# Performance work log

Hardware: AMD Instinct MI355X
Metric: run time of the kernel (lower is better)

Reference implementation:

```python
import jax, jax.numpy as jnp
import numpy as np

GROUPSIZE = 4      # g: multivariate group size (d = groupsize - 2)
NB_GROUPS = 48     # f: number of expert groups / filters
CHANNELS = 128     # c: signal channels fed to the L operator
SCALE = 0.999
SLOPE = 1.0        # model_params['scaling']
LAMB_INIT = 0.1
EPS_OMEGA_INIT = -2.0


def proj_l1(x):
    """Euclidean projection onto the unit l1 ball along axis 1. x: [B,G,F,H,W]."""
    ax = jnp.abs(x)
    s = -jnp.sort(-ax, axis=1)                      # descending |x|
    cssv = jnp.cumsum(s, axis=1) - 1.0
    G = x.shape[1]
    k = jnp.arange(1, G + 1, dtype=x.dtype).reshape(1, G, 1, 1, 1)
    cond = s * k > cssv
    rho = jnp.sum(cond, axis=1, keepdims=True)       # number of active coords
    theta = jnp.take_along_axis(cssv, rho - 1, axis=1) / rho.astype(x.dtype)
    theta = jnp.maximum(theta, 0.0)
    proj = jnp.sign(x) * jnp.maximum(ax - theta, 0.0)
    inside = jnp.sum(ax, axis=1, keepdims=True) <= 1.0
    return jnp.where(inside, x, proj)


def _forward(x_noisy, sigma, Q_param, taus_param, lamb, eps_omega,
             mu_w1, mu_b1, mu_w2, mu_b2, mu_w3, mu_b3, Wf, n_iter):
    lamb_e = jnp.exp(lamb)
    eps_e = jnp.exp(eps_omega)

    # --- Q normalization + spectral norms (cached once per forward) ---
    Q = Q_param / jnp.maximum(jnp.sum(jnp.abs(Q_param), axis=2, keepdims=True), 1.0)
    Q_norms = jnp.linalg.svd(Q, compute_uv=False)[:, 0].reshape(-1, 1, 1)  # [F,1,1]
    Q_eff = Q / Q_norms ** 2
    taus = jnp.exp(jax.nn.relu(taus_param))          # [1,1,F,1,1]

    # --- per-batch noise-adaptive scaling via small MLP ---
    h = jax.nn.relu((sigma * 20.0 - 2.0) @ mu_w1 + mu_b1)
    h = jax.nn.relu(h @ mu_w2 + mu_b2)
    h = h @ mu_w3 + mu_b3                            # [B,F]
    scaling = jax.nn.relu(h * 0.05 + sigma) * SLOPE + 1e-9
    scaling = scaling.reshape(-1, 1, scaling.shape[-1], 1, 1)  # [B,1,F,1,1]

    def moreau(x):
        g = proj_l1(x)
        cost = jnp.max(jnp.abs(x - g), axis=1) + 0.5 * jnp.sum(g * g, axis=1)
        cost = cost[:, None]                         # [B,1,F,H,W]
        g = g + eps_e * x
        cost = cost + eps_e * 0.5 * jnp.sqrt(jnp.sum(x * x, axis=1, keepdims=True))
        return g, cost

    def activation(x):
        gc, cc = moreau(x)
        # orient: scale * einsum('flg,bgfhw->blfhw', Q/Q_norms^2, x), then /taus
        y = SCALE * jnp.einsum('flg,bgfhw->blfhw', Q_eff, x) / taus
        gcc, ccc = moreau(y)
        # unorient: scale * einsum with Q^T  (Q^T[f,l,g] = Q[f,g,l])
        gcc = SCALE * jnp.einsum('fgl,bgfhw->blfhw', Q, gcc)
        ccc = Q_norms ** 2 * (taus * ccc)
        return lamb_e * (gc - gcc), lamb_e * (cc - ccc)

    def reconstruct(x):
        Lx = jnp.einsum('gfc,bchw->bgfhw', Wf, x) / scaling
        g, cost = activation(Lx)
        g = jnp.einsum('gfc,bgfhw->bchw', Wf, g * scaling)   # adjoint L^T
        cost = jnp.sum(cost * scaling ** 2, axis=(1, 2, 3, 4))
        g = (x - x_noisy + g) / (1.0 + lamb_e * (1.0 + eps_e))
        cost = cost + 0.5 * jnp.sum((x - x_noisy) ** 2, axis=(1, 2, 3))
        return g, cost

    def step(x, _):
        g, _c = reconstruct(x)
        return x - g, None

    x_final, _ = jax.lax.scan(jax.checkpoint(step), x_noisy, jnp.arange(n_iter))
    return x_final


def setup_inputs() -> dict:
    key = jax.random.key(0)
    ks = jax.random.split(key, 8)
    B, C, H, W = 2, CHANNELS, 128, 128
    F_, G = NB_GROUPS, GROUPSIZE
    x_noisy = jax.random.normal(ks[0], (B, C, H, W), jnp.float32)
    sigma = jax.random.uniform(ks[1], (B, 1), jnp.float32)
    Q_param = jax.random.uniform(ks[2], (F_, G, G), jnp.float32) - 0.5
    taus_param = (LAMB_INIT / 2.0) * jnp.ones((1, 1, F_, 1, 1), jnp.float32)
    lamb = jnp.float32(LAMB_INIT)
    eps_omega = jnp.float32(EPS_OMEGA_INIT)
    mu_w1 = jax.random.normal(ks[3], (1, F_), jnp.float32)
    mu_b1 = jnp.zeros((F_,), jnp.float32)
    mu_w2 = jax.random.normal(ks[4], (F_, F_), jnp.float32) / np.float32(np.sqrt(F_))
    mu_b2 = jnp.zeros((F_,), jnp.float32)
    mu_w3 = jax.random.normal(ks[5], (F_, F_), jnp.float32) / np.float32(np.sqrt(F_))
    mu_b3 = jnp.zeros((F_,), jnp.float32)
    Wf = jax.random.normal(ks[6], (G, F_, C), jnp.float32) / np.float32(np.sqrt(C))
    return dict(x_noisy=x_noisy, sigma=sigma, Q_param=Q_param, taus_param=taus_param,
                lamb=lamb, eps_omega=eps_omega, mu_w1=mu_w1, mu_b1=mu_b1,
                mu_w2=mu_w2, mu_b2=mu_b2, mu_w3=mu_w3, mu_b3=mu_b3, Wf=Wf, n_iter=10)


def reference(x_noisy, sigma, Q_param, taus_param, lamb, eps_omega,
              mu_w1, mu_b1, mu_w2, mu_b2, mu_w3, mu_b3, Wf, n_iter):
    return _forward(x_noisy, sigma, Q_param, taus_param, lamb, eps_omega,
                    mu_w1, mu_b1, mu_w2, mu_b2, mu_w3, mu_b3, Wf, n_iter)
```

## Files before the change

kernel.cpp:

```cpp
#include <hip/hip_runtime.h>
#include <math.h>

#define F_ 48
#define C_ 128
#define HW 16384
#define SCALE_C 0.999f
#define TPB 256

typedef __attribute__((ext_vector_type(8))) short short8;
typedef __attribute__((ext_vector_type(4))) float floatx4;

#define P1_U 0
#define P2_U 98304
#define QEQN_F 98304
#define MISC_F (QEQN_F + 1536)
#define SINV_F (MISC_F + 2)
#define SLAM_F (SINV_F + 96)

#define XS 152
#define AS 104
#define QS 36

__device__ __forceinline__ unsigned short f2bf(float f) {
    unsigned u = __float_as_uint(f);
    unsigned r = u + 0x7fffu + ((u >> 16) & 1u);
    return (unsigned short)(r >> 16);
}
__device__ __forceinline__ float bf2f(unsigned short h) {
    return __uint_as_float(((unsigned)h) << 16);
}

__global__ void setup_math(const float* __restrict__ sigma,
                           const float* __restrict__ Qp,
                           const float* __restrict__ taus_p,
                           const float* __restrict__ lamb,
                           const float* __restrict__ eps_om,
                           const float* __restrict__ mw1, const float* __restrict__ mb1,
                           const float* __restrict__ mw2, const float* __restrict__ mb2,
                           const float* __restrict__ mw3, const float* __restrict__ mb3,
                           float* __restrict__ wsf)
{
    const int tid = threadIdx.x;
    if (tid < F_) {
        const int f = tid;
        float Qm[4][4];
        for (int g = 0; g < 4; ++g) {
            float s = 0.f;
            for (int l = 0; l < 4; ++l) s += fabsf(Qp[f * 16 + g * 4 + l]);
            float d = fmaxf(s, 1.0f);
            for (int l = 0; l < 4; ++l) Qm[g][l] = Qp[f * 16 + g * 4 + l] / d;
        }
        double A[4][4];
        for (int i = 0; i < 4; ++i)
            for (int j = 0; j < 4; ++j) {
                double s = 0.0;
                for (int g = 0; g < 4; ++g) s += (double)Qm[g][i] * (double)Qm[g][j];
                A[i][j] = s;
            }
        double M[4][4];
        for (int i = 0; i < 4; ++i) for (int j = 0; j < 4; ++j) M[i][j] = A[i][j];
        for (int it = 0; it < 30; ++it) {
            double T[4][4]; double mx = 0.0;
            for (int i = 0; i < 4; ++i)
                for (int j = 0; j < 4; ++j) {
                    double s = 0.0;
                    for (int k = 0; k < 4; ++k) s += M[i][k] * M[k][j];
                    T[i][j] = s;
                    double a = fabs(s); if (a > mx) mx = a;
                }
            if (mx < 1e-300) break;
            double inv = 1.0 / mx;
            for (int i = 0; i < 4; ++i) for (int j = 0; j < 4; ++j) M[i][j] = T[i][j] * inv;
        }
        int jb = 0; double bn = -1.0;
        for (int j = 0; j < 4; ++j) {
            double nn = 0.0;
            for (int i = 0; i < 4; ++i) nn += M[i][j] * M[i][j];
            if (nn > bn) { bn = nn; jb = j; }
        }
        double v[4]; for (int i = 0; i < 4; ++i) v[i] = M[i][jb];
        double Av[4];
        for (int i = 0; i < 4; ++i) {
            double s = 0.0;
            for (int j = 0; j < 4; ++j) s += A[i][j] * v[j];
            Av[i] = s;
        }
        double vv = 0.0, vav = 0.0;
        for (int i = 0; i < 4; ++i) { vv += v[i] * v[i]; vav += v[i] * Av[i]; }
        float lamf = (float)((vv > 0.0) ? (vav / vv) : 0.0);
        float tau = expf(fmaxf(taus_p[f], 0.0f));
        float qsv = SCALE_C / tau;
        for (int l = 0; l < 4; ++l)
            for (int g = 0; g < 4; ++g)
                wsf[QEQN_F + f * 32 + l * 4 + g] = qsv * Qm[l][g] / lamf;
        for (int g = 0; g < 4; ++g)
            for (int l = 0; l < 4; ++l)
                wsf[QEQN_F + f * 32 + 16 + g * 4 + l] = SCALE_C * Qm[g][l];
    }
    if (tid >= 48 && tid < 50) {
        const int b = tid - 48;
        float lamb_e = expf(lamb[0]);
        float sg = sigma[b];
        float t = sg * 20.0f - 2.0f;
        float h1[F_], h2[F_];
        for (int j = 0; j < F_; ++j) h1[j] = fmaxf(t * mw1[j] + mb1[j], 0.0f);
        for (int j = 0; j < F_; ++j) {
            float s = mb2[j];
            for (int k = 0; k < F_; ++k) s += h1[k] * mw2[k * F_ + j];
            h2[j] = fmaxf(s, 0.0f);
        }
        for (int j = 0; j < F_; ++j) {
            float s = mb3[j];
            for (int k = 0; k < F_; ++k) s += h2[k] * mw3[k * F_ + j];
            float sc = fmaxf(s * 0.05f + sg, 0.0f) + 1e-9f;
            wsf[SINV_F + b * F_ + j] = 1.0f / sc;
            wsf[SLAM_F + b * F_ + j] = lamb_e * sc;
        }
    }
    if (tid == 50) {
        float lamb_e = expf(lamb[0]);
        float eps_e = expf(eps_om[0]);
        wsf[MISC_F + 0] = eps_e;
        wsf[MISC_F + 1] = 1.0f / (1.0f + lamb_e * (1.0f + eps_e));
    }
}

__global__ void setup_pack(const float* __restrict__ Wf, float* __restrict__ wsf)
{
    unsigned short* wsu = (unsigned short*)wsf;
    const int gtid = blockIdx.x * TPB + threadIdx.x;
    for (int i = gtid; i < 49152; i += gridDim.x * TPB) {
        if (i < 24576) {
            int j = i & 7, lane = (i >> 3) & 63;
            int t = i >> 9;
            int ks = t & 3, mt = t >> 2;
            int m = lane & 15, q = lane >> 4;
            int r = mt * 16 + m;
            int c = ks * 32 + q * 8 + j;
            int f = r >> 2, g = r & 3;
            float w = Wf[(g * F_ + f) * C_ + c];
#pragma unroll
            for (int b = 0; b < 2; ++b) {
                float v = w * wsf[SINV_F + b * F_ + f];
                unsigned short h = (unsigned short)(__float_as_uint(v) >> 16);
                float lo = v - bf2f(h);
                unsigned short l = (unsigned short)(__float_as_uint(lo) >> 16);
                wsu[P1_U + ((((b * 2 + 0) * 12 + mt) * 4 + ks) * 64 + lane) * 8 + j] = h;
                wsu[P1_U + ((((b * 2 + 1) * 12 + mt) * 4 + ks) * 64 + lane) * 8 + j] = l;
            }
        } else {
            int ii = i - 24576;
            int j = ii & 7, lane = (ii >> 3) & 63;
            int t = ii >> 9;
            int ks = t % 6, cmt = t / 6;
            int m = lane & 15, q = lane >> 4;
            int cch = cmt * 16 + m;
            int r = ks * 32 + q * 8 + j;
            int f = r >> 2, g = r & 3;
            float w = Wf[(g * F_ + f) * C_ + cch];
#pragma unroll
            for (int b = 0; b < 2; ++b) {
                float v = w * wsf[SLAM_F + b * F_ + f];
                unsigned short h = (unsigned short)(__float_as_uint(v) >> 16);
                float lo = v - bf2f(h);
                unsigned short l = (unsigned short)(__float_as_uint(lo) >> 16);
                wsu[P2_U + ((((b * 2 + 0) * 8 + cmt) * 6 + ks) * 64 + lane) * 8 + j] = h;
                wsu[P2_U + ((((b * 2 + 1) * 8 + cmt) * 6 + ks) * 64 + lane) * 8 + j] = l;
            }
        }
    }
}

__device__ __forceinline__ void proj4(const float v[4], float o[4]) {
    float a0 = fabsf(v[0]), a1 = fabsf(v[1]), a2 = fabsf(v[2]), a3 = fabsf(v[3]);
    float sum = a0 + a1 + a2 + a3;
    float t0 = fmaxf(a0, a1), u0 = fminf(a0, a1);
    float t1 = fmaxf(a2, a3), u1 = fminf(a2, a3);
    float s0 = fmaxf(t0, t1), m0 = fminf(t0, t1);
    float m1 = fmaxf(u0, u1), s3 = fminf(u0, u1);
    float s1 = fmaxf(m1, m0), s2 = fminf(m1, m0);
    float c2 = s0 + s1, c3 = c2 + s2, c4 = c3 + s3;
    float th = s0 - 1.0f, rh = 1.0f;
    if (s1 * 2.0f > c2 - 1.0f) { th = c2 - 1.0f; rh = 2.0f; }
    if (s2 * 3.0f > c3 - 1.0f) { th = c3 - 1.0f; rh = 3.0f; }
    if (s3 * 4.0f > c4 - 1.0f) { th = c4 - 1.0f; rh = 4.0f; }
    float theta = fmaxf(th / rh, 0.0f);
    bool inside = (sum <= 1.0f);
#pragma unroll
    for (int g = 0; g < 4; ++g) {
        float ag = fabsf(v[g]);
        float pg = copysignf(fmaxf(ag - theta, 0.0f), v[g]);
        o[g] = inside ? v[g] : pg;
    }
}

__global__ __launch_bounds__(TPB, 4) void mfoe_main(
    const float* __restrict__ xnoisy,
    const float* __restrict__ wsf,
    float* __restrict__ out,
    const int* __restrict__ n_iter_p)
{
    __shared__ __align__(16) unsigned short sXH[32 * XS];
    __shared__ __align__(16) unsigned short sXL[32 * XS];
    __shared__ __align__(16) unsigned short sACT[32 * AS];
    __shared__ __align__(16) float sQ[F_ * QS];

    const int tid = threadIdx.x;
    const int lane = tid & 63;
    const int wv = __builtin_amdgcn_readfirstlane(tid >> 6);
    const int n = lane & 15;
    const int q = lane >> 4;
    const int blk = blockIdx.x;
    const int b = blk >> 9;
    const int pix0 = (blk & 511) << 5;

    const float* __restrict__ xin = xnoisy + b * (C_ * HW) + pix0;
    float* __restrict__ oimg = out + b * (C_ * HW) + pix0;
    const unsigned short* __restrict__ wsu = (const unsigned short*)wsf;
    const int niter = *n_iter_p;

    if (niter == 0) {
        for (int i = tid; i < C_ * 32; i += TPB) {
            int p = i & 31, c = i >> 5;
            oimg[c * HW + p] = xin[c * HW + p];
        }
        return;
    }

    for (int i = tid; i < C_ * 32; i += TPB) {
        int p = i & 31, c = i >> 5;
        float v = xin[c * HW + p];
        unsigned short h = (unsigned short)(__float_as_uint(v) >> 16);
        float lo = v - bf2f(h);
        sXH[p * XS + c] = h;
        sXL[p * XS + c] = (unsigned short)(__float_as_uint(lo) >> 16);
    }
    for (int i = tid; i < F_ * 32; i += TPB)
        sQ[(i >> 5) * QS + (i & 31)] = wsf[QEQN_F + i];

    float xnr[16];
#pragma unroll
    for (int j = 0; j < 4; ++j) {
        int jw = wv * 4 + j, cmt = jw >> 1, nt = jw & 1;
        int p = nt * 16 + n;
#pragma unroll
        for (int reg = 0; reg < 4; ++reg)
            xnr[j * 4 + reg] = xin[(cmt * 16 + q * 4 + reg) * HW + p];
    }
    const float eps_e = wsf[MISC_F + 0];
    const float invden = wsf[MISC_F + 1];

    for (int it = 0; it < niter; ++it) {
        floatx4 acc2[4];
#pragma unroll
        for (int j = 0; j < 4; ++j) acc2[j] = (floatx4){0.f, 0.f, 0.f, 0.f};

#pragma unroll 1
        for (int h = 0; h < 2; ++h) {
            __syncthreads();
#pragma unroll 1
            for (int j = 0; j < 3; ++j) {
                int jw = wv * 3 + j, mtl = jw >> 1, nt = jw & 1;
                int mt = h * 6 + mtl;
                int p = nt * 16 + n;
                floatx4 acc = (floatx4){0.f, 0.f, 0.f, 0.f};
                const short8* aHp = (const short8*)(wsu + P1_U + (((b * 2 + 0) * 12 + mt) * 4) * 512 + lane * 8);
                const short8* aLp = (const short8*)(wsu + P1_U + (((b * 2 + 1) * 12 + mt) * 4) * 512 + lane * 8);
#pragma unroll
                for (int ks = 0; ks < 4; ++ks) {
                    short8 aH = aHp[ks * 64];
                    short8 aL = aLp[ks * 64];
                    short8 bH = *(const short8*)&sXH[p * XS + ks * 32 + q * 8];
                    short8 bL = *(const short8*)&sXL[p * XS + ks * 32 + q * 8];
                    acc = __builtin_amdgcn_mfma_f32_16x16x32_bf16(aH, bH, acc, 0, 0, 0);
                    acc = __builtin_amdgcn_mfma_f32_16x16x32_bf16(aH, bL, acc, 0, 0, 0);
                    acc = __builtin_amdgcn_mfma_f32_16x16x32_bf16(aL, bH, acc, 0, 0, 0);
                }
                int f = h * 24 + mtl * 4 + q;
                float qv[32];
#pragma unroll
                for (int k = 0; k < 8; ++k)
                    *(floatx4*)&qv[4 * k] = *(const floatx4*)&sQ[f * QS + 4 * k];
                float v[4] = {acc[0], acc[1], acc[2], acc[3]};
                float pv[4]; proj4(v, pv);
                float y[4];
#pragma unroll
                for (int l = 0; l < 4; ++l)
                    y[l] = fmaf(qv[l * 4 + 0], v[0], fmaf(qv[l * 4 + 1], v[1],
                           fmaf(qv[l * 4 + 2], v[2], qv[l * 4 + 3] * v[3])));
                float py[4]; proj4(y, py);
                float m2[4];
#pragma unroll
                for (int g = 0; g < 4; ++g) m2[g] = fmaf(eps_e, y[g], py[g]);
                unsigned pk0, pk1;
                {
                    float a0, a1;
                    float gcc0 = fmaf(qv[16 + 0], m2[0], fmaf(qv[16 + 4], m2[1],
                                 fmaf(qv[16 + 8], m2[2], qv[16 + 12] * m2[3])));
                    a0 = fmaf(eps_e, v[0], pv[0]) - gcc0;
                    float gcc1 = fmaf(qv[17 + 0], m2[0], fmaf(qv[17 + 4], m2[1],
                                 fmaf(qv[17 + 8], m2[2], qv[17 + 12] * m2[3])));
                    a1 = fmaf(eps_e, v[1], pv[1]) - gcc1;
                    pk0 = ((unsigned)f2bf(a1) << 16) | f2bf(a0);
                    float gcc2 = fmaf(qv[18 + 0], m2[0], fmaf(qv[18 + 4], m2[1],
                                 fmaf(qv[18 + 8], m2[2], qv[18 + 12] * m2[3])));
                    a0 = fmaf(eps_e, v[2], pv[2]) - gcc2;
                    float gcc3 = fmaf(qv[19 + 0], m2[0], fmaf(qv[19 + 4], m2[1],
                                 fmaf(qv[19 + 8], m2[2], qv[19 + 12] * m2[3])));
                    a1 = fmaf(eps_e, v[3], pv[3]) - gcc3;
                    pk1 = ((unsigned)f2bf(a1) << 16) | f2bf(a0);
                }
                unsigned long long pk = ((unsigned long long)pk1 << 32) | pk0;
                *(unsigned long long*)&sACT[p * AS + mtl * 16 + q * 4] = pk;
            }
            __syncthreads();
#pragma unroll
            for (int j = 0; j < 4; ++j) {
                int jw = wv * 4 + j, cmt = jw >> 1, nt = jw & 1;
                int p = nt * 16 + n;
                const short8* a2H = (const short8*)(wsu + P2_U + (((b * 2 + 0) * 8 + cmt) * 6 + h * 3) * 512 + lane * 8);
                const short8* a2L = (const short8*)(wsu + P2_U + (((b * 2 + 1) * 8 + cmt) * 6 + h * 3) * 512 + lane * 8);
                floatx4 a = acc2[j];
#pragma unroll
                for (int ksl = 0; ksl < 3; ++ksl) {
                    short8 aH = a2H[ksl * 64];
                    short8 aL = a2L[ksl * 64];
                    short8 bA = *(const short8*)&sACT[p * AS + ksl * 32 + q * 8];
                    a = __builtin_amdgcn_mfma_f32_16x16x32_bf16(aH, bA, a, 0, 0, 0);
                    a = __builtin_amdgcn_mfma_f32_16x16x32_bf16(aL, bA, a, 0, 0, 0);
                }
                acc2[j] = a;
            }
        }
        const bool last = (it == niter - 1);
#pragma unroll
        for (int j = 0; j < 4; ++j) {
            int jw = wv * 4 + j, cmt = jw >> 1, nt = jw & 1;
            int p = nt * 16 + n;
            int cb = cmt * 16 + q * 4;
            unsigned long long oh = *(const unsigned long long*)&sXH[p * XS + cb];
            unsigned long long ol = *(const unsigned long long*)&sXL[p * XS + cb];
            unsigned long long nh = 0ull, nl = 0ull;
#pragma unroll
            for (int reg = 0; reg < 4; ++reg) {
                float xo = bf2f((unsigned short)(oh >> (16 * reg))) +
                           bf2f((unsigned short)(ol >> (16 * reg)));
                float nx = xo - (xo - xnr[j * 4 + reg] + acc2[j][reg]) * invden;
                if (last) oimg[(cb + reg) * HW + p] = nx;
                unsigned short hh = (unsigned short)(__float_as_uint(nx) >> 16);
                float lo = nx - bf2f(hh);
                unsigned short ll = (unsigned short)(__float_as_uint(lo) >> 16);
                nh |= ((unsigned long long)hh) << (16 * reg);
                nl |= ((unsigned long long)ll) << (16 * reg);
            }
            *(unsigned long long*)&sXH[p * XS + cb] = nh;
            *(unsigned long long*)&sXL[p * XS + cb] = nl;
        }
    }
}

extern "C" void kernel_launch(void* const* d_in, const int* in_sizes, int n_in,
                              void* d_out, int out_size, void* d_ws, size_t ws_size,
                              hipStream_t stream) {
    const float* x_noisy = (const float*)d_in[0];
    const float* sigma   = (const float*)d_in[1];
    const float* Qp      = (const float*)d_in[2];
    const float* taus_p  = (const float*)d_in[3];
    const float* lamb    = (const float*)d_in[4];
    const float* eps_om  = (const float*)d_in[5];
    const float* mw1     = (const float*)d_in[6];
    const float* mb1     = (const float*)d_in[7];
    const float* mw2     = (const float*)d_in[8];
    const float* mb2     = (const float*)d_in[9];
    const float* mw3     = (const float*)d_in[10];
    const float* mb3     = (const float*)d_in[11];
    const float* Wf      = (const float*)d_in[12];
    const int*   n_iter  = (const int*)d_in[13];
    float* out = (float*)d_out;
    float* ws  = (float*)d_ws;

    hipLaunchKernelGGL(setup_math, dim3(1), dim3(64), 0, stream,
                       sigma, Qp, taus_p, lamb, eps_om,
                       mw1, mb1, mw2, mb2, mw3, mb3, ws);
    hipLaunchKernelGGL(setup_pack, dim3(192), dim3(TPB), 0, stream, Wf, ws);
    hipLaunchKernelGGL(mfoe_main, dim3(1024), dim3(TPB), 0, stream,
                       x_noisy, ws, out, n_iter);
}
```

Baseline: 333.1 us.

## Merge setup kernels and process all filter groups in one activation pass

Two setup kernels are merged into one. Each block recomputes the small per-batch MLP scaling into shared memory, and block 0 alone writes the Q tables, which removes one launch. In the main loop the split over two halves of the 48 filters is removed. All 12 M-tiles are computed into a wider activation buffer in LDS (AS 104→200), followed by a single 6-step K loop for the second GEMM. This cuts barriers per iteration from four to two, at the cost of more LDS per block, which may lower occupancy.

Result: slower. 452.4 us (+35.8%).

```diff
diff --git a/kernel.cpp b/kernel.cpp
--- a/kernel.cpp
+++ b/kernel.cpp
@@ -9,16 +9,14 @@
 
 typedef __attribute__((ext_vector_type(8))) short short8;
 typedef __attribute__((ext_vector_type(4))) float floatx4;
+typedef __attribute__((ext_vector_type(2))) unsigned int uint2v;
 
 #define P1_U 0
 #define P2_U 98304
 #define QEQN_F 98304
 #define MISC_F (QEQN_F + 1536)
-#define SINV_F (MISC_F + 2)
-#define SLAM_F (SINV_F + 96)
-
 #define XS 152
-#define AS 104
+#define AS 200
 #define QS 36
 
 __device__ __forceinline__ unsigned short f2bf(float f) {
@@ -30,73 +28,22 @@
     return __uint_as_float(((unsigned)h) << 16);
 }
 
-__global__ void setup_math(const float* __restrict__ sigma,
-                           const float* __restrict__ Qp,
-                           const float* __restrict__ taus_p,
-                           const float* __restrict__ lamb,
-                           const float* __restrict__ eps_om,
-                           const float* __restrict__ mw1, const float* __restrict__ mb1,
-                           const float* __restrict__ mw2, const float* __restrict__ mb2,
-                           const float* __restrict__ mw3, const float* __restrict__ mb3,
-                           float* __restrict__ wsf)
+__global__ void setup_all(const float* __restrict__ sigma,
+                          const float* __restrict__ Qp,
+                          const float* __restrict__ taus_p,
+                          const float* __restrict__ lamb,
+                          const float* __restrict__ eps_om,
+                          const float* __restrict__ mw1, const float* __restrict__ mb1,
+                          const float* __restrict__ mw2, const float* __restrict__ mb2,
+                          const float* __restrict__ mw3, const float* __restrict__ mb3,
+                          const float* __restrict__ Wf,
+                          float* __restrict__ wsf)
 {
+    __shared__ float sInv[2][F_];
+    __shared__ float sLam[2][F_];
     const int tid = threadIdx.x;
-    if (tid < F_) {
-        const int f = tid;
-        float Qm[4][4];
-        for (int g = 0; g < 4; ++g) {
-            float s = 0.f;
-            for (int l = 0; l < 4; ++l) s += fabsf(Qp[f * 16 + g * 4 + l]);
-            float d = fmaxf(s, 1.0f);
-            for (int l = 0; l < 4; ++l) Qm[g][l] = Qp[f * 16 + g * 4 + l] / d;
-        }
-        double A[4][4];
-        for (int i = 0; i < 4; ++i)
-            for (int j = 0; j < 4; ++j) {
-                double s = 0.0;
-                for (int g = 0; g < 4; ++g) s += (double)Qm[g][i] * (double)Qm[g][j];
-                A[i][j] = s;
-            }
-        double M[4][4];
-        for (int i = 0; i < 4; ++i) for (int j = 0; j < 4; ++j) M[i][j] = A[i][j];
-        for (int it = 0; it < 30; ++it) {
-            double T[4][4]; double mx = 0.0;
-            for (int i = 0; i < 4; ++i)
-                for (int j = 0; j < 4; ++j) {
-                    double s = 0.0;
-                    for (int k = 0; k < 4; ++k) s += M[i][k] * M[k][j];
-                    T[i][j] = s;
-                    double a = fabs(s); if (a > mx) mx = a;
-                }
-            if (mx < 1e-300) break;
-            double inv = 1.0 / mx;
-            for (int i = 0; i < 4; ++i) for (int j = 0; j < 4; ++j) M[i][j] = T[i][j] * inv;
-        }
-        int jb = 0; double bn = -1.0;
-        for (int j = 0; j < 4; ++j) {
-            double nn = 0.0;
-            for (int i = 0; i < 4; ++i) nn += M[i][j] * M[i][j];
-            if (nn > bn) { bn = nn; jb = j; }
-        }
-        double v[4]; for (int i = 0; i < 4; ++i) v[i] = M[i][jb];
-        double Av[4];
-        for (int i = 0; i < 4; ++i) {
-            double s = 0.0;
-            for (int j = 0; j < 4; ++j) s += A[i][j] * v[j];
-            Av[i] = s;
-        }
-        double vv = 0.0, vav = 0.0;
-        for (int i = 0; i < 4; ++i) { vv += v[i] * v[i]; vav += v[i] * Av[i]; }
-        float lamf = (float)((vv > 0.0) ? (vav / vv) : 0.0);
-        float tau = expf(fmaxf(taus_p[f], 0.0f));
-        float qsv = SCALE_C / tau;
-        for (int l = 0; l < 4; ++l)
-            for (int g = 0; g < 4; ++g)
-                wsf[QEQN_F + f * 32 + l * 4 + g] = qsv * Qm[l][g] / lamf;
-        for (int g = 0; g < 4; ++g)
-            for (int l = 0; l < 4; ++l)
-                wsf[QEQN_F + f * 32 + 16 + g * 4 + l] = SCALE_C * Qm[g][l];
-    }
+    unsigned short* wsu = (unsigned short*)wsf;
+
     if (tid >= 48 && tid < 50) {
         const int b = tid - 48;
         float lamb_e = expf(lamb[0]);
@@ -113,23 +60,77 @@
             float s = mb3[j];
             for (int k = 0; k < F_; ++k) s += h2[k] * mw3[k * F_ + j];
             float sc = fmaxf(s * 0.05f + sg, 0.0f) + 1e-9f;
-            wsf[SINV_F + b * F_ + j] = 1.0f / sc;
-            wsf[SLAM_F + b * F_ + j] = lamb_e * sc;
-        }
-    }
-    if (tid == 50) {
-        float lamb_e = expf(lamb[0]);
-        float eps_e = expf(eps_om[0]);
-        wsf[MISC_F + 0] = eps_e;
-        wsf[MISC_F + 1] = 1.0f / (1.0f + lamb_e * (1.0f + eps_e));
-    }
-}
-
-__global__ void setup_pack(const float* __restrict__ Wf, float* __restrict__ wsf)
-{
-    unsigned short* wsu = (unsigned short*)wsf;
-    const int gtid = blockIdx.x * TPB + threadIdx.x;
-    for (int i = gtid; i < 49152; i += gridDim.x * TPB) {
+            sInv[b][j] = 1.0f / sc;
+            sLam[b][j] = lamb_e * sc;
+        }
+    }
+    if (blockIdx.x == 0) {
+        if (tid < F_) {
+            const int f = tid;
+            float Qm[4][4];
+            for (int g = 0; g < 4; ++g) {
+                float s = 0.f;
+                for (int l = 0; l < 4; ++l) s += fabsf(Qp[f * 16 + g * 4 + l]);
+                float d = fmaxf(s, 1.0f);
+                for (int l = 0; l < 4; ++l) Qm[g][l] = Qp[f * 16 + g * 4 + l] / d;
+            }
+            double A[4][4];
+            for (int i = 0; i < 4; ++i)
+                for (int j = 0; j < 4; ++j) {
+                    double s = 0.0;
+                    for (int g = 0; g < 4; ++g) s += (double)Qm[g][i] * (double)Qm[g][j];
+                    A[i][j] = s;
+                }
+            double M[4][4];
+            for (int i = 0; i < 4; ++i) for (int j = 0; j < 4; ++j) M[i][j] = A[i][j];
+            for (int it = 0; it < 30; ++it) {
+                double T[4][4]; double mx = 0.0;
+                for (int i = 0; i < 4; ++i)
+                    for (int j = 0; j < 4; ++j) {
+                        double s = 0.0;
+                        for (int k = 0; k < 4; ++k) s += M[i][k] * M[k][j];
+                        T[i][j] = s;
+                        double a = fabs(s); if (a > mx) mx = a;
+                    }
+                if (mx < 1e-300) break;
+                double inv = 1.0 / mx;
+                for (int i = 0; i < 4; ++i) for (int j = 0; j < 4; ++j) M[i][j] = T[i][j] * inv;
+            }
+            int jb = 0; double bn = -1.0;
+            for (int j = 0; j < 4; ++j) {
+                double nn = 0.0;
+                for (int i = 0; i < 4; ++i) nn += M[i][j] * M[i][j];
+                if (nn > bn) { bn = nn; jb = j; }
+            }
+            double v[4]; for (int i = 0; i < 4; ++i) v[i] = M[i][jb];
+            double Av[4];
+            for (int i = 0; i < 4; ++i) {
+                double s = 0.0;
+                for (int j = 0; j < 4; ++j) s += A[i][j] * v[j];
+                Av[i] = s;
+            }
+            double vv = 0.0, vav = 0.0;
+            for (int i = 0; i < 4; ++i) { vv += v[i] * v[i]; vav += v[i] * Av[i]; }
+            float lamf = (float)((vv > 0.0) ? (vav / vv) : 0.0);
+            float tau = expf(fmaxf(taus_p[f], 0.0f));
+            float qsv = SCALE_C / tau;
+            for (int l = 0; l < 4; ++l)
+                for (int g = 0; g < 4; ++g)
+                    wsf[QEQN_F + f * 32 + l * 4 + g] = qsv * Qm[l][g] / lamf;
+            for (int g = 0; g < 4; ++g)
+                for (int l = 0; l < 4; ++l)
+                    wsf[QEQN_F + f * 32 + 16 + g * 4 + l] = SCALE_C * Qm[g][l];
+        }
+        if (tid == 50) {
+            float lamb_e = expf(lamb[0]);
+            float eps_e = expf(eps_om[0]);
+            wsf[MISC_F + 0] = eps_e;
+            wsf[MISC_F + 1] = 1.0f / (1.0f + lamb_e * (1.0f + eps_e));
+        }
+    }
+    __syncthreads();
+
+    for (int i = blockIdx.x * TPB + tid; i < 49152; i += gridDim.x * TPB) {
         if (i < 24576) {
             int j = i & 7, lane = (i >> 3) & 63;
             int t = i >> 9;
@@ -141,7 +142,7 @@
             float w = Wf[(g * F_ + f) * C_ + c];
 #pragma unroll
             for (int b = 0; b < 2; ++b) {
-                float v = w * wsf[SINV_F + b * F_ + f];
+                float v = w * sInv[b][f];
                 unsigned short h = (unsigned short)(__float_as_uint(v) >> 16);
                 float lo = v - bf2f(h);
                 unsigned short l = (unsigned short)(__float_as_uint(lo) >> 16);
@@ -160,7 +161,7 @@
             float w = Wf[(g * F_ + f) * C_ + cch];
 #pragma unroll
             for (int b = 0; b < 2; ++b) {
-                float v = w * wsf[SLAM_F + b * F_ + f];
+                float v = w * sLam[b][f];
                 unsigned short h = (unsigned short)(__float_as_uint(v) >> 16);
                 float lo = v - bf2f(h);
                 unsigned short l = (unsigned short)(__float_as_uint(lo) >> 16);
@@ -251,86 +252,80 @@
     const float invden = wsf[MISC_F + 1];
 
     for (int it = 0; it < niter; ++it) {
+        __syncthreads();
+#pragma unroll 1
+        for (int j = 0; j < 6; ++j) {
+            int jw = wv * 6 + j, mt = jw >> 1, nt = jw & 1;
+            int p = nt * 16 + n;
+            floatx4 acc = (floatx4){0.f, 0.f, 0.f, 0.f};
+            const short8* aHp = (const short8*)(wsu + P1_U + (((b * 2 + 0) * 12 + mt) * 4) * 512 + lane * 8);
+            const short8* aLp = (const short8*)(wsu + P1_U + (((b * 2 + 1) * 12 + mt) * 4) * 512 + lane * 8);
+#pragma unroll
+            for (int ks = 0; ks < 4; ++ks) {
+                short8 aH = aHp[ks * 64];
+                short8 aL = aLp[ks * 64];
+                short8 bH = *(const short8*)&sXH[p * XS + ks * 32 + q * 8];
+                short8 bL = *(const short8*)&sXL[p * XS + ks * 32 + q * 8];
+                acc = __builtin_amdgcn_mfma_f32_16x16x32_bf16(aH, bH, acc, 0, 0, 0);
+                acc = __builtin_amdgcn_mfma_f32_16x16x32_bf16(aH, bL, acc, 0, 0, 0);
+                acc = __builtin_amdgcn_mfma_f32_16x16x32_bf16(aL, bH, acc, 0, 0, 0);
+            }
+            int f = mt * 4 + q;
+            float qv[32];
+#pragma unroll
+            for (int k = 0; k < 8; ++k)
+                *(floatx4*)&qv[4 * k] = *(const floatx4*)&sQ[f * QS + 4 * k];
+            float v[4] = {acc[0], acc[1], acc[2], acc[3]};
+            float pv[4]; proj4(v, pv);
+            float y[4];
+#pragma unroll
+            for (int l = 0; l < 4; ++l)
+                y[l] = fmaf(qv[l * 4 + 0], v[0], fmaf(qv[l * 4 + 1], v[1],
+                       fmaf(qv[l * 4 + 2], v[2], qv[l * 4 + 3] * v[3])));
+            float py[4]; proj4(y, py);
+            float m2[4];
+#pragma unroll
+            for (int g = 0; g < 4; ++g) m2[g] = fmaf(eps_e, y[g], py[g]);
+            unsigned pk0, pk1;
+            {
+                float a0, a1;
+                float gcc0 = fmaf(qv[16 + 0], m2[0], fmaf(qv[16 + 4], m2[1],
+                             fmaf(qv[16 + 8], m2[2], qv[16 + 12] * m2[3])));
+                a0 = fmaf(eps_e, v[0], pv[0]) - gcc0;
+                float gcc1 = fmaf(qv[17 + 0], m2[0], fmaf(qv[17 + 4], m2[1],
+                             fmaf(qv[17 + 8], m2[2], qv[17 + 12] * m2[3])));
+                a1 = fmaf(eps_e, v[1], pv[1]) - gcc1;
+                pk0 = ((unsigned)f2bf(a1) << 16) | f2bf(a0);
+                float gcc2 = fmaf(qv[18 + 0], m2[0], fmaf(qv[18 + 4], m2[1],
+                             fmaf(qv[18 + 8], m2[2], qv[18 + 12] * m2[3])));
+                a0 = fmaf(eps_e, v[2], pv[2]) - gcc2;
+                float gcc3 = fmaf(qv[19 + 0], m2[0], fmaf(qv[19 + 4], m2[1],
+                             fmaf(qv[19 + 8], m2[2], qv[19 + 12] * m2[3])));
+                a1 = fmaf(eps_e, v[3], pv[3]) - gcc3;
+                pk1 = ((unsigned)f2bf(a1) << 16) | f2bf(a0);
+            }
+            *(uint2v*)&sACT[p * AS + mt * 16 + q * 4] = (uint2v){pk0, pk1};
+        }
+        __syncthreads();
         floatx4 acc2[4];
 #pragma unroll
         for (int j = 0; j < 4; ++j) acc2[j] = (floatx4){0.f, 0.f, 0.f, 0.f};
-
-#pragma unroll 1
-        for (int h = 0; h < 2; ++h) {
-            __syncthreads();
-#pragma unroll 1
-            for (int j = 0; j < 3; ++j) {
-                int jw = wv * 3 + j, mtl = jw >> 1, nt = jw & 1;
-                int mt = h * 6 + mtl;
-                int p = nt * 16 + n;
-                floatx4 acc = (floatx4){0.f, 0.f, 0.f, 0.f};
-                const short8* aHp = (const short8*)(wsu + P1_U + (((b * 2 + 0) * 12 + mt) * 4) * 512 + lane * 8);
-                const short8* aLp = (const short8*)(wsu + P1_U + (((b * 2 + 1) * 12 + mt) * 4) * 512 + lane * 8);
-#pragma unroll
-                for (int ks = 0; ks < 4; ++ks) {
-                    short8 aH = aHp[ks * 64];
-                    short8 aL = aLp[ks * 64];
-                    short8 bH = *(const short8*)&sXH[p * XS + ks * 32 + q * 8];
-                    short8 bL = *(const short8*)&sXL[p * XS + ks * 32 + q * 8];
-                    acc = __builtin_amdgcn_mfma_f32_16x16x32_bf16(aH, bH, acc, 0, 0, 0);
-                    acc = __builtin_amdgcn_mfma_f32_16x16x32_bf16(aH, bL, acc, 0, 0, 0);
-                    acc = __builtin_amdgcn_mfma_f32_16x16x32_bf16(aL, bH, acc, 0, 0, 0);
-                }
-                int f = h * 24 + mtl * 4 + q;
-                float qv[32];
-#pragma unroll
-                for (int k = 0; k < 8; ++k)
-                    *(floatx4*)&qv[4 * k] = *(const floatx4*)&sQ[f * QS + 4 * k];
-                float v[4] = {acc[0], acc[1], acc[2], acc[3]};
-                float pv[4]; proj4(v, pv);
-                float y[4];
-#pragma unroll
-                for (int l = 0; l < 4; ++l)
-                    y[l] = fmaf(qv[l * 4 + 0], v[0], fmaf(qv[l * 4 + 1], v[1],
-                           fmaf(qv[l * 4 + 2], v[2], qv[l * 4 + 3] * v[3])));
-                float py[4]; proj4(y, py);
-                float m2[4];
-#pragma unroll
-                for (int g = 0; g < 4; ++g) m2[g] = fmaf(eps_e, y[g], py[g]);
-                unsigned pk0, pk1;
-                {
-                    float a0, a1;
-                    float gcc0 = fmaf(qv[16 + 0], m2[0], fmaf(qv[16 + 4], m2[1],
-                                 fmaf(qv[16 + 8], m2[2], qv[16 + 12] * m2[3])));
-                    a0 = fmaf(eps_e, v[0], pv[0]) - gcc0;
-                    float gcc1 = fmaf(qv[17 + 0], m2[0], fmaf(qv[17 + 4], m2[1],
-                                 fmaf(qv[17 + 8], m2[2], qv[17 + 12] * m2[3])));
-                    a1 = fmaf(eps_e, v[1], pv[1]) - gcc1;
-                    pk0 = ((unsigned)f2bf(a1) << 16) | f2bf(a0);
-                    float gcc2 = fmaf(qv[18 + 0], m2[0], fmaf(qv[18 + 4], m2[1],
-                                 fmaf(qv[18 + 8], m2[2], qv[18 + 12] * m2[3])));
-                    a0 = fmaf(eps_e, v[2], pv[2]) - gcc2;
-                    float gcc3 = fmaf(qv[19 + 0], m2[0], fmaf(qv[19 + 4], m2[1],
-                                 fmaf(qv[19 + 8], m2[2], qv[19 + 12] * m2[3])));
-                    a1 = fmaf(eps_e, v[3], pv[3]) - gcc3;
-                    pk1 = ((unsigned)f2bf(a1) << 16) | f2bf(a0);
-                }
-                unsigned long long pk = ((unsigned long long)pk1 << 32) | pk0;
-                *(unsigned long long*)&sACT[p * AS + mtl * 16 + q * 4] = pk;
-            }
-            __syncthreads();
-#pragma unroll
-            for (int j = 0; j < 4; ++j) {
-                int jw = wv * 4 + j, cmt = jw >> 1, nt = jw & 1;
-                int p = nt * 16 + n;
-                const short8* a2H = (const short8*)(wsu + P2_U + (((b * 2 + 0) * 8 + cmt) * 6 + h * 3) * 512 + lane * 8);
-                const short8* a2L = (const short8*)(wsu + P2_U + (((b * 2 + 1) * 8 + cmt) * 6 + h * 3) * 512 + lane * 8);
-                floatx4 a = acc2[j];
-#pragma unroll
-                for (int ksl = 0; ksl < 3; ++ksl) {
-                    short8 aH = a2H[ksl * 64];
-                    short8 aL = a2L[ksl * 64];
-                    short8 bA = *(const short8*)&sACT[p * AS + ksl * 32 + q * 8];
-                    a = __builtin_amdgcn_mfma_f32_16x16x32_bf16(aH, bA, a, 0, 0, 0);
-                    a = __builtin_amdgcn_mfma_f32_16x16x32_bf16(aL, bA, a, 0, 0, 0);
-                }
-                acc2[j] = a;
-            }
+#pragma unroll
+        for (int j = 0; j < 4; ++j) {
+            int jw = wv * 4 + j, cmt = jw >> 1, nt = jw & 1;
+            int p = nt * 16 + n;
+            const short8* a2H = (const short8*)(wsu + P2_U + (((b * 2 + 0) * 8 + cmt) * 6) * 512 + lane * 8);
+            const short8* a2L = (const short8*)(wsu + P2_U + (((b * 2 + 1) * 8 + cmt) * 6) * 512 + lane * 8);
+            floatx4 a = acc2[j];
+#pragma unroll
+            for (int ks = 0; ks < 6; ++ks) {
+                short8 aH = a2H[ks * 64];
+                short8 aL = a2L[ks * 64];
+                short8 bA = *(const short8*)&sACT[p * AS + ks * 32 + q * 8];
+                a = __builtin_amdgcn_mfma_f32_16x16x32_bf16(aH, bA, a, 0, 0, 0);
+                a = __builtin_amdgcn_mfma_f32_16x16x32_bf16(aL, bA, a, 0, 0, 0);
+            }
+            acc2[j] = a;
         }
         const bool last = (it == niter - 1);
 #pragma unroll
@@ -379,10 +374,9 @@
     float* out = (float*)d_out;
     float* ws  = (float*)d_ws;
 
-    hipLaunchKernelGGL(setup_math, dim3(1), dim3(64), 0, stream,
+    hipLaunchKernelGGL(setup_all, dim3(64), dim3(TPB), 0, stream,
                        sigma, Qp, taus_p, lamb, eps_om,
-                       mw1, mb1, mw2, mb2, mw3, mb3, ws);
-    hipLaunchKernelGGL(setup_pack, dim3(192), dim3(TPB), 0, stream, Wf, ws);
+                       mw1, mb1, mw2, mb2, mw3, mb3, Wf, ws);
     hipLaunchKernelGGL(mfoe_main, dim3(1024), dim3(TPB), 0, stream,
                        x_noisy, ws, out, n_iter);
 }
```
